# Optimization experiments

Hardware: AMD Instinct MI355X
Metric: run time of the kernel (lower is better)

## Reference

```python
import jax, jax.numpy as jnp
import numpy as np

BN_EPS = 1e-5


def setup_inputs() -> dict:
    key = jax.random.key(0)
    ks = jax.random.split(key, 13)
    B, C, H, W = 32, 256, 96, 48
    return {
        "x": jax.random.normal(ks[0], (B, C, H, W), dtype=jnp.float32),
        "g_w": jax.random.normal(ks[1], (C,), dtype=jnp.float32),
        "g_b": jax.random.normal(ks[2], (1,), dtype=jnp.float32),
        "theta_w": jax.random.normal(ks[3], (C,), dtype=jnp.float32),
        "theta_b": jax.random.normal(ks[4], (1,), dtype=jnp.float32),
        "phi_w": jax.random.normal(ks[5], (C,), dtype=jnp.float32),
        "phi_b": jax.random.normal(ks[6], (1,), dtype=jnp.float32),
        "W_w": jax.random.normal(ks[7], (C,), dtype=jnp.float32),
        "W_b": jax.random.normal(ks[8], (C,), dtype=jnp.float32),
        "bn_gamma": jax.random.normal(ks[9], (C,), dtype=jnp.float32),
        "bn_beta": jax.random.normal(ks[10], (C,), dtype=jnp.float32),
        "bn_mean": jax.random.normal(ks[11], (C,), dtype=jnp.float32),
        "bn_var": jax.random.uniform(ks[12], (C,), dtype=jnp.float32),
    }


def reference(x, g_w, g_b, theta_w, theta_b, phi_w, phi_b, W_w, W_b,
              bn_gamma, bn_beta, bn_mean, bn_var):
    # x: (B, C, H, W); inter_channels == 1 so all 1x1 convs are channel dots.
    B, C, H, Wd = x.shape
    N = H * Wd
    xf = x.reshape(B, C, N)  # (B, C, N)

    g = jnp.einsum("c,bcn->bn", g_w, xf) + g_b          # (B, N)
    theta = jnp.einsum("c,bcn->bn", theta_w, xf) + theta_b
    phi = jnp.einsum("c,bcn->bn", phi_w, xf) + phi_b

    # f_div_C @ g_x == theta * (phi . g) / N  (rank-1 contraction, exact by associativity)
    s = jnp.sum(phi * g, axis=1) / N                     # (B,)
    y = theta * s[:, None]                               # (B, N), inter_channels dim is 1

    # W: 1x1 conv 1->C, then BatchNorm (inference form), then residual add.
    Wy = y[:, None, :] * W_w[None, :, None] + W_b[None, :, None]  # (B, C, N)
    inv_std = bn_gamma / jnp.sqrt(bn_var + BN_EPS)                 # (C,)
    bn = (Wy - bn_mean[None, :, None]) * inv_std[None, :, None] + bn_beta[None, :, None]

    z = bn.reshape(B, C, H, Wd) + x
    return z
```

## Files before the change

kernel.cpp:

```cpp
#include <hip/hip_runtime.h>

constexpr int Bn = 32;
constexpr int Cn = 256;
constexpr int Hn = 96;
constexpr int Wn = 48;
constexpr int Nn = Hn * Wn;
constexpr int N4 = Nn / 4;
constexpr int TILES = 72;
constexpr int NBLK  = Bn * TILES;
constexpr float BN_EPS = 1e-5f;

typedef float floatx4 __attribute__((ext_vector_type(4)));

__global__ __launch_bounds__(128, 5) void pass1_kernel(
    const float* __restrict__ x,
    const float* __restrict__ g_w, const float* __restrict__ g_b,
    const float* __restrict__ theta_w, const float* __restrict__ theta_b,
    const float* __restrict__ phi_w, const float* __restrict__ phi_b,
    float* __restrict__ theta_out,
    float* __restrict__ part_out)
{
    __shared__ float wg[Cn], wt[Cn], wp[Cn];
    __shared__ float4 xw_g[16], xw_t[16], xw_p[16];

    const int tid  = threadIdx.x;
    const int lane = tid & 63;
    const int wave = tid >> 6;
    const int pos  = tid & 15;
    const int grp  = tid >> 4;

    #pragma unroll
    for (int i = tid; i < Cn; i += 128) {
        wg[i] = g_w[i];
        wt[i] = theta_w[i];
        wp[i] = phi_w[i];
    }
    __syncthreads();

    const int bx   = blockIdx.x;
    const int b    = bx / TILES;
    const int tile = bx - b * TILES;
    const int n4   = tile * 16 + pos;

    const float4* xb = reinterpret_cast<const float4*>(x)
                     + (size_t)b * (size_t)(Cn * N4) + n4;

    float4 ag = {0.f, 0.f, 0.f, 0.f};
    float4 at = {0.f, 0.f, 0.f, 0.f};
    float4 ap = {0.f, 0.f, 0.f, 0.f};

    const int c0 = grp * 32;
    #pragma unroll
    for (int k = 0; k < 4; ++k) {
        float4 buf[8];
        #pragma unroll
        for (int i = 0; i < 8; ++i)
            buf[i] = xb[(size_t)(c0 + k * 8 + i) * N4];
        #pragma unroll
        for (int i = 0; i < 8; ++i) {
            const int c = c0 + k * 8 + i;
            const float cg = wg[c], ct = wt[c], cp = wp[c];
            const float4 xv = buf[i];
            ag.x = fmaf(cg, xv.x, ag.x);
            ag.y = fmaf(cg, xv.y, ag.y);
            ag.z = fmaf(cg, xv.z, ag.z);
            ag.w = fmaf(cg, xv.w, ag.w);
            at.x = fmaf(ct, xv.x, at.x);
            at.y = fmaf(ct, xv.y, at.y);
            at.z = fmaf(ct, xv.z, at.z);
            at.w = fmaf(ct, xv.w, at.w);
            ap.x = fmaf(cp, xv.x, ap.x);
            ap.y = fmaf(cp, xv.y, ap.y);
            ap.z = fmaf(cp, xv.z, ap.z);
            ap.w = fmaf(cp, xv.w, ap.w);
        }
    }

    ag.x += __shfl_xor(ag.x, 16); ag.y += __shfl_xor(ag.y, 16);
    ag.z += __shfl_xor(ag.z, 16); ag.w += __shfl_xor(ag.w, 16);
    at.x += __shfl_xor(at.x, 16); at.y += __shfl_xor(at.y, 16);
    at.z += __shfl_xor(at.z, 16); at.w += __shfl_xor(at.w, 16);
    ap.x += __shfl_xor(ap.x, 16); ap.y += __shfl_xor(ap.y, 16);
    ap.z += __shfl_xor(ap.z, 16); ap.w += __shfl_xor(ap.w, 16);

    ag.x += __shfl_xor(ag.x, 32); ag.y += __shfl_xor(ag.y, 32);
    ag.z += __shfl_xor(ag.z, 32); ag.w += __shfl_xor(ag.w, 32);
    at.x += __shfl_xor(at.x, 32); at.y += __shfl_xor(at.y, 32);
    at.z += __shfl_xor(at.z, 32); at.w += __shfl_xor(at.w, 32);
    ap.x += __shfl_xor(ap.x, 32); ap.y += __shfl_xor(ap.y, 32);
    ap.z += __shfl_xor(ap.z, 32); ap.w += __shfl_xor(ap.w, 32);

    if (wave == 1 && lane < 16) {
        xw_g[pos] = ag;
        xw_t[pos] = at;
        xw_p[pos] = ap;
    }
    __syncthreads();

    if (wave == 0 && lane < 16) {
        const float4 rg = xw_g[pos];
        const float4 rt = xw_t[pos];
        const float4 rp = xw_p[pos];
        float4 sg = {ag.x + rg.x, ag.y + rg.y, ag.z + rg.z, ag.w + rg.w};
        float4 st = {at.x + rt.x, at.y + rt.y, at.z + rt.z, at.w + rt.w};
        float4 sp = {ap.x + rp.x, ap.y + rp.y, ap.z + rp.z, ap.w + rp.w};

        const float gb = g_b[0], tb = theta_b[0], pb = phi_b[0];

        float4 th;
        th.x = st.x + tb; th.y = st.y + tb; th.z = st.z + tb; th.w = st.w + tb;
        reinterpret_cast<float4*>(theta_out)[(size_t)b * N4 + n4] = th;

        float p = (sg.x + gb) * (sp.x + pb)
                + (sg.y + gb) * (sp.y + pb)
                + (sg.z + gb) * (sp.z + pb)
                + (sg.w + gb) * (sp.w + pb);

        p += __shfl_down(p, 8);
        p += __shfl_down(p, 4);
        p += __shfl_down(p, 2);
        p += __shfl_down(p, 1);

        if (pos == 0)
            part_out[b * TILES + tile] = p;
    }
}

__global__ __launch_bounds__(128, 5) void pass2_kernel(
    const float* __restrict__ x,
    const float* __restrict__ theta_buf,
    const float* __restrict__ part_buf,
    const float* __restrict__ W_w, const float* __restrict__ W_b,
    const float* __restrict__ bn_gamma, const float* __restrict__ bn_beta,
    const float* __restrict__ bn_mean, const float* __restrict__ bn_var,
    float* __restrict__ out)
{
    __shared__ float a_sh[Cn], d_sh[Cn];
    __shared__ float s_sh;

    const int tid  = threadIdx.x;
    const int pos  = tid & 15;
    const int grp  = tid >> 4;

    const int bx   = (NBLK - 1) - blockIdx.x;
    const int b    = bx / TILES;
    const int tile = bx - b * TILES;
    const int n4   = tile * 16 + pos;

    #pragma unroll
    for (int i = tid; i < Cn; i += 128) {
        const float inv_std = bn_gamma[i] * rsqrtf(bn_var[i] + BN_EPS);
        a_sh[i] = W_w[i] * inv_std;
        d_sh[i] = fmaf(W_b[i] - bn_mean[i], inv_std, bn_beta[i]);
    }

    if (tid < 64) {
        float p = part_buf[b * TILES + tid];
        if (tid < TILES - 64)
            p += part_buf[b * TILES + 64 + tid];
        p += __shfl_down(p, 32);
        p += __shfl_down(p, 16);
        p += __shfl_down(p, 8);
        p += __shfl_down(p, 4);
        p += __shfl_down(p, 2);
        p += __shfl_down(p, 1);
        if (tid == 0) s_sh = p * (1.0f / (float)Nn);
    }
    __syncthreads();
    const float sb = s_sh;

    const float4 th = reinterpret_cast<const float4*>(theta_buf)[(size_t)b * N4 + n4];
    const float tsx = th.x * sb, tsy = th.y * sb,
                tsz = th.z * sb, tsw = th.w * sb;

    const float4* xb = reinterpret_cast<const float4*>(x)
                     + (size_t)b * (size_t)(Cn * N4) + n4;
    floatx4* ob = reinterpret_cast<floatx4*>(out)
                + (size_t)b * (size_t)(Cn * N4) + n4;

    const int c0 = grp * 32;
    #pragma unroll
    for (int k = 0; k < 4; ++k) {
        float4 buf[8];
        #pragma unroll
        for (int i = 0; i < 8; ++i)
            buf[i] = xb[(size_t)(c0 + k * 8 + i) * N4];
        #pragma unroll
        for (int i = 0; i < 8; ++i) {
            const int c = c0 + k * 8 + i;
            const float a = a_sh[c];
            const float d = d_sh[c];
            const float4 xv = buf[i];

            floatx4 o;
            o.x = fmaf(tsx, a, d) + xv.x;
            o.y = fmaf(tsy, a, d) + xv.y;
            o.z = fmaf(tsz, a, d) + xv.z;
            o.w = fmaf(tsw, a, d) + xv.w;

            __builtin_nontemporal_store(o, &ob[(size_t)c * N4]);
        }
    }
}

extern "C" void kernel_launch(void* const* d_in, const int* in_sizes, int n_in,
                              void* d_out, int out_size, void* d_ws, size_t ws_size,
                              hipStream_t stream) {
    const float* x        = (const float*)d_in[0];
    const float* g_w      = (const float*)d_in[1];
    const float* g_b      = (const float*)d_in[2];
    const float* theta_w  = (const float*)d_in[3];
    const float* theta_b  = (const float*)d_in[4];
    const float* phi_w    = (const float*)d_in[5];
    const float* phi_b    = (const float*)d_in[6];
    const float* W_w      = (const float*)d_in[7];
    const float* W_b      = (const float*)d_in[8];
    const float* bn_gamma = (const float*)d_in[9];
    const float* bn_beta  = (const float*)d_in[10];
    const float* bn_mean  = (const float*)d_in[11];
    const float* bn_var   = (const float*)d_in[12];

    float* out = (float*)d_out;

    float* part_buf  = (float*)d_ws;
    float* theta_buf = (float*)((char*)d_ws + 16384);

    pass1_kernel<<<NBLK, 128, 0, stream>>>(
        x, g_w, g_b, theta_w, theta_b, phi_w, phi_b, theta_buf, part_buf);

    pass2_kernel<<<NBLK, 128, 0, stream>>>(
        x, theta_buf, part_buf, W_w, W_b,
        bn_gamma, bn_beta, bn_mean, bn_var, out);
}
```

Measured before the change: 74.68 us.

## Fuse both passes into one kernel with a per-batch atomic barrier

Merges the projection/partial-sum pass and the output pass into a single kernel. Each block keeps its x tile in registers, 16 float4 per thread, across 256 threads. It publishes its partial phi·g sum, then spins on a per-batch atomic counter until all 72 tiles of that batch have arrived. This removes the second full read of x and the theta round trip through global memory. In exchange it adds a memset launch, spin-wait latency, higher register pressure, and depends on every block of a batch eventually being scheduled while others spin.

```diff
diff --git a/kernel.cpp b/kernel.cpp
--- a/kernel.cpp
+++ b/kernel.cpp
@@ -12,16 +12,24 @@
 
 typedef float floatx4 __attribute__((ext_vector_type(4)));
 
-__global__ __launch_bounds__(128, 5) void pass1_kernel(
+__global__ __launch_bounds__(256, 3) void fused_kernel(
     const float* __restrict__ x,
     const float* __restrict__ g_w, const float* __restrict__ g_b,
     const float* __restrict__ theta_w, const float* __restrict__ theta_b,
     const float* __restrict__ phi_w, const float* __restrict__ phi_b,
-    float* __restrict__ theta_out,
-    float* __restrict__ part_out)
+    const float* __restrict__ W_w, const float* __restrict__ W_b,
+    const float* __restrict__ bn_gamma, const float* __restrict__ bn_beta,
+    const float* __restrict__ bn_mean, const float* __restrict__ bn_var,
+    int*   __restrict__ counters,
+    float* __restrict__ part_buf,
+    float* __restrict__ out)
 {
     __shared__ float wg[Cn], wt[Cn], wp[Cn];
-    __shared__ float4 xw_g[16], xw_t[16], xw_p[16];
+    __shared__ float a_sh[Cn], d_sh[Cn];
+    __shared__ float4 red_g[3][16], red_t[3][16], red_p[3][16];
+    __shared__ float4 theta_sh[16];
+    __shared__ float part_sh[TILES];
+    __shared__ float s_sh;
 
     const int tid  = threadIdx.x;
     const int lane = tid & 63;
@@ -29,51 +37,51 @@
     const int pos  = tid & 15;
     const int grp  = tid >> 4;
 
-    #pragma unroll
-    for (int i = tid; i < Cn; i += 128) {
-        wg[i] = g_w[i];
-        wt[i] = theta_w[i];
-        wp[i] = phi_w[i];
-    }
-    __syncthreads();
-
     const int bx   = blockIdx.x;
     const int b    = bx / TILES;
     const int tile = bx - b * TILES;
     const int n4   = tile * 16 + pos;
 
+    wg[tid] = g_w[tid];
+    wt[tid] = theta_w[tid];
+    wp[tid] = phi_w[tid];
+    {
+        const float inv_std = bn_gamma[tid] * rsqrtf(bn_var[tid] + BN_EPS);
+        a_sh[tid] = W_w[tid] * inv_std;
+        d_sh[tid] = fmaf(W_b[tid] - bn_mean[tid], inv_std, bn_beta[tid]);
+    }
+    __syncthreads();
+
     const float4* xb = reinterpret_cast<const float4*>(x)
                      + (size_t)b * (size_t)(Cn * N4) + n4;
+    const int c0 = grp * 16;
+
+    float4 xr[16];
+    #pragma unroll
+    for (int i = 0; i < 16; ++i)
+        xr[i] = xb[(size_t)(c0 + i) * N4];
 
     float4 ag = {0.f, 0.f, 0.f, 0.f};
     float4 at = {0.f, 0.f, 0.f, 0.f};
     float4 ap = {0.f, 0.f, 0.f, 0.f};
 
-    const int c0 = grp * 32;
     #pragma unroll
-    for (int k = 0; k < 4; ++k) {
-        float4 buf[8];
-        #pragma unroll
-        for (int i = 0; i < 8; ++i)
-            buf[i] = xb[(size_t)(c0 + k * 8 + i) * N4];
-        #pragma unroll
-        for (int i = 0; i < 8; ++i) {
-            const int c = c0 + k * 8 + i;
-            const float cg = wg[c], ct = wt[c], cp = wp[c];
-            const float4 xv = buf[i];
-            ag.x = fmaf(cg, xv.x, ag.x);
-            ag.y = fmaf(cg, xv.y, ag.y);
-            ag.z = fmaf(cg, xv.z, ag.z);
-            ag.w = fmaf(cg, xv.w, ag.w);
-            at.x = fmaf(ct, xv.x, at.x);
-            at.y = fmaf(ct, xv.y, at.y);
-            at.z = fmaf(ct, xv.z, at.z);
-            at.w = fmaf(ct, xv.w, at.w);
-            ap.x = fmaf(cp, xv.x, ap.x);
-            ap.y = fmaf(cp, xv.y, ap.y);
-            ap.z = fmaf(cp, xv.z, ap.z);
-            ap.w = fmaf(cp, xv.w, ap.w);
-        }
+    for (int i = 0; i < 16; ++i) {
+        const int c = c0 + i;
+        const float cg = wg[c], ct = wt[c], cp = wp[c];
+        const float4 xv = xr[i];
+        ag.x = fmaf(cg, xv.x, ag.x);
+        ag.y = fmaf(cg, xv.y, ag.y);
+        ag.z = fmaf(cg, xv.z, ag.z);
+        ag.w = fmaf(cg, xv.w, ag.w);
+        at.x = fmaf(ct, xv.x, at.x);
+        at.y = fmaf(ct, xv.y, at.y);
+        at.z = fmaf(ct, xv.z, at.z);
+        at.w = fmaf(ct, xv.w, at.w);
+        ap.x = fmaf(cp, xv.x, ap.x);
+        ap.y = fmaf(cp, xv.y, ap.y);
+        ap.z = fmaf(cp, xv.z, ap.z);
+        ap.w = fmaf(cp, xv.w, ap.w);
     }
 
     ag.x += __shfl_xor(ag.x, 16); ag.y += __shfl_xor(ag.y, 16);
@@ -90,26 +98,30 @@
     ap.x += __shfl_xor(ap.x, 32); ap.y += __shfl_xor(ap.y, 32);
     ap.z += __shfl_xor(ap.z, 32); ap.w += __shfl_xor(ap.w, 32);
 
-    if (wave == 1 && lane < 16) {
-        xw_g[pos] = ag;
-        xw_t[pos] = at;
-        xw_p[pos] = ap;
+    if (wave > 0 && lane < 16) {
+        red_g[wave - 1][pos] = ag;
+        red_t[wave - 1][pos] = at;
+        red_p[wave - 1][pos] = ap;
     }
     __syncthreads();
 
     if (wave == 0 && lane < 16) {
-        const float4 rg = xw_g[pos];
-        const float4 rt = xw_t[pos];
-        const float4 rp = xw_p[pos];
-        float4 sg = {ag.x + rg.x, ag.y + rg.y, ag.z + rg.z, ag.w + rg.w};
-        float4 st = {at.x + rt.x, at.y + rt.y, at.z + rt.z, at.w + rt.w};
-        float4 sp = {ap.x + rp.x, ap.y + rp.y, ap.z + rp.z, ap.w + rp.w};
+        float4 sg = ag, st = at, sp = ap;
+        #pragma unroll
+        for (int w = 0; w < 3; ++w) {
+            const float4 rg = red_g[w][pos];
+            const float4 rt = red_t[w][pos];
+            const float4 rp = red_p[w][pos];
+            sg.x += rg.x; sg.y += rg.y; sg.z += rg.z; sg.w += rg.w;
+            st.x += rt.x; st.y += rt.y; st.z += rt.z; st.w += rt.w;
+            sp.x += rp.x; sp.y += rp.y; sp.z += rp.z; sp.w += rp.w;
+        }
 
         const float gb = g_b[0], tb = theta_b[0], pb = phi_b[0];
 
         float4 th;
         th.x = st.x + tb; th.y = st.y + tb; th.z = st.z + tb; th.w = st.w + tb;
-        reinterpret_cast<float4*>(theta_out)[(size_t)b * N4 + n4] = th;
+        theta_sh[pos] = th;
 
         float p = (sg.x + gb) * (sp.x + pb)
                 + (sg.y + gb) * (sp.y + pb)
@@ -121,43 +133,33 @@
         p += __shfl_down(p, 2);
         p += __shfl_down(p, 1);
 
-        if (pos == 0)
-            part_out[b * TILES + tile] = p;
-    }
-}
-
-__global__ __launch_bounds__(128, 5) void pass2_kernel(
-    const float* __restrict__ x,
-    const float* __restrict__ theta_buf,
-    const float* __restrict__ part_buf,
-    const float* __restrict__ W_w, const float* __restrict__ W_b,
-    const float* __restrict__ bn_gamma, const float* __restrict__ bn_beta,
-    const float* __restrict__ bn_mean, const float* __restrict__ bn_var,
-    float* __restrict__ out)
-{
-    __shared__ float a_sh[Cn], d_sh[Cn];
-    __shared__ float s_sh;
-
-    const int tid  = threadIdx.x;
-    const int pos  = tid & 15;
-    const int grp  = tid >> 4;
-
-    const int bx   = (NBLK - 1) - blockIdx.x;
-    const int b    = bx / TILES;
-    const int tile = bx - b * TILES;
-    const int n4   = tile * 16 + pos;
-
-    #pragma unroll
-    for (int i = tid; i < Cn; i += 128) {
-        const float inv_std = bn_gamma[i] * rsqrtf(bn_var[i] + BN_EPS);
-        a_sh[i] = W_w[i] * inv_std;
-        d_sh[i] = fmaf(W_b[i] - bn_mean[i], inv_std, bn_beta[i]);
-    }
+        if (pos == 0) {
+            __hip_atomic_store(&part_buf[b * TILES + tile], p,
+                               __ATOMIC_RELAXED, __HIP_MEMORY_SCOPE_AGENT);
+            __hip_atomic_fetch_add(&counters[b], 1,
+                                   __ATOMIC_RELEASE, __HIP_MEMORY_SCOPE_AGENT);
+        }
+    }
+
+    if (tid == 0) {
+        while (__hip_atomic_load(&counters[b], __ATOMIC_RELAXED,
+                                 __HIP_MEMORY_SCOPE_AGENT) < TILES)
+            __builtin_amdgcn_s_sleep(2);
+        (void)__hip_atomic_load(&counters[b], __ATOMIC_ACQUIRE,
+                                __HIP_MEMORY_SCOPE_AGENT);
+    }
+    __syncthreads();
+
+    if (tid < TILES)
+        part_sh[tid] = __hip_atomic_load(&part_buf[b * TILES + tid],
+                                         __ATOMIC_RELAXED,
+                                         __HIP_MEMORY_SCOPE_AGENT);
+    __syncthreads();
 
     if (tid < 64) {
-        float p = part_buf[b * TILES + tid];
+        float p = part_sh[tid];
         if (tid < TILES - 64)
-            p += part_buf[b * TILES + 64 + tid];
+            p += part_sh[64 + tid];
         p += __shfl_down(p, 32);
         p += __shfl_down(p, 16);
         p += __shfl_down(p, 8);
@@ -169,37 +171,27 @@
     __syncthreads();
     const float sb = s_sh;
 
-    const float4 th = reinterpret_cast<const float4*>(theta_buf)[(size_t)b * N4 + n4];
+    const float4 th = theta_sh[pos];
     const float tsx = th.x * sb, tsy = th.y * sb,
                 tsz = th.z * sb, tsw = th.w * sb;
 
-    const float4* xb = reinterpret_cast<const float4*>(x)
-                     + (size_t)b * (size_t)(Cn * N4) + n4;
     floatx4* ob = reinterpret_cast<floatx4*>(out)
                 + (size_t)b * (size_t)(Cn * N4) + n4;
 
-    const int c0 = grp * 32;
     #pragma unroll
-    for (int k = 0; k < 4; ++k) {
-        float4 buf[8];
-        #pragma unroll
-        for (int i = 0; i < 8; ++i)
-            buf[i] = xb[(size_t)(c0 + k * 8 + i) * N4];
-        #pragma unroll
-        for (int i = 0; i < 8; ++i) {
-            const int c = c0 + k * 8 + i;
-            const float a = a_sh[c];
-            const float d = d_sh[c];
-            const float4 xv = buf[i];
-
-            floatx4 o;
-            o.x = fmaf(tsx, a, d) + xv.x;
-            o.y = fmaf(tsy, a, d) + xv.y;
-            o.z = fmaf(tsz, a, d) + xv.z;
-            o.w = fmaf(tsw, a, d) + xv.w;
-
-            __builtin_nontemporal_store(o, &ob[(size_t)c * N4]);
-        }
+    for (int i = 0; i < 16; ++i) {
+        const int c = c0 + i;
+        const float a = a_sh[c];
+        const float d = d_sh[c];
+        const float4 xv = xr[i];
+
+        floatx4 o;
+        o.x = fmaf(tsx, a, d) + xv.x;
+        o.y = fmaf(tsy, a, d) + xv.y;
+        o.z = fmaf(tsz, a, d) + xv.z;
+        o.w = fmaf(tsw, a, d) + xv.w;
+
+        __builtin_nontemporal_store(o, &ob[(size_t)c * N4]);
     }
 }
 
@@ -222,13 +214,12 @@
 
     float* out = (float*)d_out;
 
-    float* part_buf  = (float*)d_ws;
-    float* theta_buf = (float*)((char*)d_ws + 16384);
-
-    pass1_kernel<<<NBLK, 128, 0, stream>>>(
-        x, g_w, g_b, theta_w, theta_b, phi_w, phi_b, theta_buf, part_buf);
-
-    pass2_kernel<<<NBLK, 128, 0, stream>>>(
-        x, theta_buf, part_buf, W_w, W_b,
-        bn_gamma, bn_beta, bn_mean, bn_var, out);
+    int*   counters = (int*)d_ws;
+    float* part_buf = (float*)((char*)d_ws + 512);
+
+    hipMemsetAsync(counters, 0, Bn * sizeof(int), stream);
+
+    fused_kernel<<<NBLK, 256, 0, stream>>>(
+        x, g_w, g_b, theta_w, theta_b, phi_w, phi_b, W_w, W_b,
+        bn_gamma, bn_beta, bn_mean, bn_var, counters, part_buf, out);
 }
```

Result: slower. 295.2 us (+295.2%).
